# Optimization experiments

Hardware: AMD Instinct MI355X
Metric: run time of the kernel (lower is better)

Reference implementation:

```python
import jax, jax.numpy as jnp
import numpy as np

B = 4096
INPUT_DIM = 4096
N_BLOCKS = 8
BLOCK = INPUT_DIM // N_BLOCKS  # 512
N_EXPERTS = 6
H = 1024   # expert_hidden
H2 = H // 2


def setup_inputs() -> dict:
    key = jax.random.key(0)
    ks = jax.random.split(key, 16)
    s = 0.02  # init scale keeps tanh/softmax in sane range
    return {
        "x":   jax.random.normal(ks[0], (B, INPUT_DIM), jnp.float32),
        # routers: per-block stacked weights [8, ...]
        "Wr1": jax.random.normal(ks[1], (N_BLOCKS, BLOCK, 32), jnp.float32) * s,
        "br1": jax.random.normal(ks[2], (N_BLOCKS, 32), jnp.float32) * s,
        "Wr2": jax.random.normal(ks[3], (N_BLOCKS, 32, N_EXPERTS), jnp.float32) * s,
        "br2": jax.random.normal(ks[4], (N_BLOCKS, N_EXPERTS), jnp.float32) * s,
        # experts: stacked [6, ...], shared across all 8 blocks
        "We1": jax.random.normal(ks[5], (N_EXPERTS, BLOCK, H), jnp.float32) * s,
        "be1": jax.random.normal(ks[6], (N_EXPERTS, H), jnp.float32) * s,
        "We2": jax.random.normal(ks[7], (N_EXPERTS, H, H2), jnp.float32) * s,
        "be2": jax.random.normal(ks[8], (N_EXPERTS, H2), jnp.float32) * s,
        "We3": jax.random.normal(ks[9], (N_EXPERTS, H2, 3), jnp.float32) * s,
        "be3": jax.random.normal(ks[10], (N_EXPERTS, 3), jnp.float32) * s,
        # aggregator
        "Wa1": jax.random.normal(ks[11], (3, 16), jnp.float32) * s,
        "ba1": jax.random.normal(ks[12], (16,), jnp.float32) * s,
        "Wa2": jax.random.normal(ks[13], (16, 3), jnp.float32) * s,
        "ba2": jax.random.normal(ks[14], (3,), jnp.float32) * s,
    }


def reference(x, Wr1, br1, Wr2, br2, We1, be1, We2, be2, We3, be3,
              Wa1, ba1, Wa2, ba2):
    b = x.shape[0]
    blocks = x.reshape(b, N_BLOCKS, BLOCK)                       # [b,s,d]
    # routers (one per block s)
    r1 = jax.nn.relu(jnp.einsum('bsd,sdh->bsh', blocks, Wr1) + br1)
    routing = jax.nn.softmax(
        jnp.einsum('bsh,she->bse', r1, Wr2) + br2, axis=-1)      # [b,s,E]
    # experts applied to every block (grouped GEMMs)
    h1 = jnp.tanh(jnp.einsum('bsd,edh->bseh', blocks, We1) + be1)        # [b,s,E,H]
    h2 = jnp.tanh(jnp.einsum('bseh,ehk->bsek', h1, We2) + be2)           # [b,s,E,H2]
    eo = jnp.einsum('bsek,eko->bseo', h2, We3) + be3                     # [b,s,E,3]
    weighted = jnp.einsum('bse,bseo->bso', routing, eo)                  # [b,s,3]
    final = weighted.mean(axis=1)                                        # mean over 8 blocks
    a1 = jax.nn.relu(final @ Wa1 + ba1)
    return a1 @ Wa2 + ba2                                                # [b,3]
```

## Files before the change

kernel.cpp:

```cpp
#include <hip/hip_runtime.h>
#include <cstdint>
#include <cstddef>

typedef __bf16 bf16;
typedef __bf16 bf16x4 __attribute__((ext_vector_type(4)));
typedef __bf16 bf16x8 __attribute__((ext_vector_type(8)));
typedef float  f32x4  __attribute__((ext_vector_type(4)));
typedef long long i64v;

#define NROWS   32768
#define DBLK    512
#define H1N     1024
#define H2N     512
#define NEXP    6
#define NBATCH  4096
#define HALL    (NEXP * H1N)
#define W2SCALE 32.0f
#define W2INV   0.03125f

__device__ __forceinline__ void gld16(const void* g, void* l) {
    __builtin_amdgcn_global_load_lds(
        (const __attribute__((address_space(1))) void*)g,
        (__attribute__((address_space(3))) void*)l, 16, 0, 0);
}

__device__ __forceinline__ float fast_tanh(float x) {
    float e = __builtin_amdgcn_exp2f(x * 2.8853900817779268f);
    float r = __builtin_amdgcn_rcpf(e + 1.0f);
    return __builtin_fmaf(-2.0f, r, 1.0f);
}

__device__ __forceinline__ float hsum16(float v) {
    v += __shfl_xor(v, 1);
    v += __shfl_xor(v, 2);
    v += __shfl_xor(v, 4);
    v += __shfl_xor(v, 8);
    return v;
}

__device__ __forceinline__ int swz(int row, int g) {
    return row * 64 + ((g ^ (row & 7)) * 8);
}
__device__ __forceinline__ int swz8(int row, int g) {
    return row * 64 + ((g ^ ((row >> 1) & 3)) << 4);
}


__global__ void cvt_bf16_kernel(const float* __restrict__ in,
                                bf16* __restrict__ out, int n4) {
    int i = blockIdx.x * blockDim.x + threadIdx.x;
    if (i >= n4) return;
    float4 v = ((const float4*)in)[i];
    bf16x4 o;
    o.x = (bf16)v.x; o.y = (bf16)v.y; o.z = (bf16)v.z; o.w = (bf16)v.w;
    ((bf16x4*)out)[i] = o;
}

__global__ __launch_bounds__(256) void transpose_cvt(
    const float* __restrict__ in, bf16* __restrict__ out, int K, int N) {
    __shared__ bf16 tile[64][66];
    int e  = blockIdx.z;
    int n0 = blockIdx.x * 64;
    int k0 = blockIdx.y * 64;
    int c  = threadIdx.x & 63;
    int rb = threadIdx.x >> 6;
    const float* src = in + (size_t)e * K * N;
    bf16* dst = out + (size_t)e * N * K;
#pragma unroll
    for (int it = 0; it < 16; ++it) {
        int k = k0 + rb + it * 4;
        int n = n0 + c;
        if (k < K && n < N) tile[rb + it * 4][c] = (bf16)src[(size_t)k * N + n];
    }
    __syncthreads();
#pragma unroll
    for (int it = 0; it < 16; ++it) {
        int n = n0 + rb + it * 4;
        int k = k0 + c;
        if (n < N && k < K) dst[(size_t)n * K + k] = tile[c][rb + it * 4];
    }
}

__global__ __launch_bounds__(256) void transpose_cvt_fp8(
    const float* __restrict__ in, uint8_t* __restrict__ out, int K, int N,
    float scale) {
    __shared__ float tile[64][65];
    int e  = blockIdx.z;
    int n0 = blockIdx.x * 64;
    int k0 = blockIdx.y * 64;
    int c  = threadIdx.x & 63;
    int rb = threadIdx.x >> 6;
    const float* src = in + (size_t)e * K * N;
    uint8_t* dst = out + (size_t)e * N * K;
#pragma unroll
    for (int it = 0; it < 16; ++it) {
        int k = k0 + rb + it * 4;
        int n = n0 + c;
        if (k < K && n < N) tile[rb + it * 4][c] = src[(size_t)k * N + n];
    }
    __syncthreads();
#pragma unroll
    for (int it = 0; it < 16; ++it) {
        int n = n0 + rb + it * 4;
        int k = k0 + c;
        if (n < N && k < K) {
            float v = tile[c][rb + it * 4] * scale;
            int p = __builtin_amdgcn_cvt_pk_fp8_f32(v, v, 0, false);
            dst[(size_t)n * K + k] = (uint8_t)(p & 0xff);
        }
    }
}

__global__ void zero_f32_kernel(float* __restrict__ p, int n) {
    int i = blockIdx.x * blockDim.x + threadIdx.x;
    if (i < n) p[i] = 0.0f;
}


__global__ __launch_bounds__(256, 2) void router_kernel(
    const bf16* __restrict__ xbf,
    const bf16* __restrict__ Wr1t,
    const float* __restrict__ br1,
    const float* __restrict__ Wr2,
    const float* __restrict__ br2,
    float* __restrict__ routing) {
    __shared__ __align__(16) bf16 sA[128 * 64];
    __shared__ __align__(16) bf16 sB[32 * 64];
    const int tid = threadIdx.x;
    const int w = tid >> 6, l = tid & 63;
    const int s  = blockIdx.y;
    const int b0 = blockIdx.x * 128;
    const int wm = w * 32;
    const int srow = l >> 3, schk = (l & 7) * 8;
    const int fr = l & 15, fq = l >> 4;
    const bf16* Ab = xbf + (size_t)s * 512;
    const bf16* Bb = Wr1t + (size_t)s * (32 * 512);

    f32x4 acc[2][2];
#pragma unroll
    for (int i = 0; i < 2; ++i)
#pragma unroll
        for (int j = 0; j < 2; ++j) acc[i][j] = (f32x4){0.f, 0.f, 0.f, 0.f};

    for (int k0 = 0; k0 < 512; k0 += 64) {
        __syncthreads();
#pragma unroll
        for (int jj = 0; jj < 4; ++jj) {
            int row = w * 32 + jj * 8;
            gld16(Ab + (size_t)(b0 + row + srow) * 4096 + k0 + schk, sA + row * 64);
        }
        gld16(Bb + (size_t)(w * 8 + srow) * 512 + k0 + schk, sB + w * 8 * 64);
        __syncthreads();
#pragma unroll
        for (int ks = 0; ks < 2; ++ks) {
            bf16x8 af[2], bfr[2];
#pragma unroll
            for (int i = 0; i < 2; ++i)
                af[i] = *(const bf16x8*)&sA[(wm + i * 16 + fr) * 64 + ks * 32 + fq * 8];
#pragma unroll
            for (int j = 0; j < 2; ++j)
                bfr[j] = *(const bf16x8*)&sB[(j * 16 + fr) * 64 + ks * 32 + fq * 8];
#pragma unroll
            for (int i = 0; i < 2; ++i)
#pragma unroll
                for (int j = 0; j < 2; ++j)
                    acc[i][j] = __builtin_amdgcn_mfma_f32_16x16x32_bf16(
                        af[i], bfr[j], acc[i][j], 0, 0, 0);
        }
    }

    float b1v[2], w2v[2][6], br2v[6];
#pragma unroll
    for (int j = 0; j < 2; ++j) {
        int col = j * 16 + fr;
        b1v[j] = br1[s * 32 + col];
#pragma unroll
        for (int e2 = 0; e2 < 6; ++e2) w2v[j][e2] = Wr2[(s * 32 + col) * 6 + e2];
    }
#pragma unroll
    for (int e2 = 0; e2 < 6; ++e2) br2v[e2] = br2[s * 6 + e2];

#pragma unroll
    for (int i = 0; i < 2; ++i) {
#pragma unroll
        for (int r = 0; r < 4; ++r) {
            float lg[6] = {0.f, 0.f, 0.f, 0.f, 0.f, 0.f};
#pragma unroll
            for (int j = 0; j < 2; ++j) {
                float t = fmaxf(acc[i][j][r] + b1v[j], 0.f);
#pragma unroll
                for (int e2 = 0; e2 < 6; ++e2) lg[e2] += t * w2v[j][e2];
            }
#pragma unroll
            for (int e2 = 0; e2 < 6; ++e2) lg[e2] = hsum16(lg[e2]) + br2v[e2];
            float mx = lg[0];
#pragma unroll
            for (int e2 = 1; e2 < 6; ++e2) mx = fmaxf(mx, lg[e2]);
            float p[6], sum = 0.f;
#pragma unroll
            for (int e2 = 0; e2 < 6; ++e2) { p[e2] = __expf(lg[e2] - mx); sum += p[e2]; }
            float inv = __fdividef(1.f, sum);
            if (fr == 0) {
                int brow = b0 + wm + i * 16 + fq * 4 + r;
                float* dst = routing + ((size_t)brow * 8 + s) * 6;
#pragma unroll
                for (int e2 = 0; e2 < 6; ++e2) dst[e2] = p[e2] * inv;
            }
        }
    }
}

__global__ __launch_bounds__(512, 2) void gemm1_kernel(
    const bf16* __restrict__ A,
    const bf16* __restrict__ B,
    const float* __restrict__ bias,
    uint8_t* __restrict__ h1,
    int ldh) {
    __shared__ __align__(16) bf16 sA[2][256 * 64];
    __shared__ __align__(16) bf16 sB[2][256 * 64];
    const int tid = threadIdx.x;
    const int w = tid >> 6, l = tid & 63;
    const int n0 = blockIdx.x * 256;
    const int m0 = blockIdx.y * 256;
    const int wm = (w & 1) * 128;
    const int wn = (w >> 1) * 64;
    const int fr = l & 15, fq = l >> 4;

    const int rbase = w * 32 + (l >> 3);
    const int gg = l & 7;
    const bf16* Ag = A + (size_t)(m0 + rbase) * DBLK + gg * 8;
    const bf16* Bg = B + (size_t)(n0 + rbase) * DBLK + gg * 8;
    const int woff = rbase * 64 + ((gg ^ (l >> 3)) * 8);

    f32x4 acc[8][4];
#pragma unroll
    for (int i = 0; i < 8; ++i)
#pragma unroll
        for (int j = 0; j < 4; ++j) acc[i][j] = (f32x4){0.f, 0.f, 0.f, 0.f};

#define G1_LOAD(SA_, SB_, T_)                                              \
    {                                                                      \
        _Pragma("unroll") for (int q = 0; q < 4; ++q) {                    \
            SA_[q] = *(const bf16x8*)(Ag + (size_t)q * 4096 + (T_) * 64);  \
            SB_[q] = *(const bf16x8*)(Bg + (size_t)q * 4096 + (T_) * 64);  \
        }                                                                  \
    }
#define G1_WRITE(SA_, SB_, BUF_)                                           \
    {                                                                      \
        _Pragma("unroll") for (int q = 0; q < 4; ++q) {                    \
            *(bf16x8*)&sA[BUF_][woff + q * 512] = SA_[q];                  \
            *(bf16x8*)&sB[BUF_][woff + q * 512] = SB_[q];                  \
        }                                                                  \
    }
#define G1_COMP(BUF_)                                                      \
    {                                                                      \
        _Pragma("unroll") for (int ks = 0; ks < 2; ++ks) {                 \
            bf16x8 af[8], bfr[4];                                          \
            _Pragma("unroll") for (int i = 0; i < 8; ++i)                  \
                af[i] = *(const bf16x8*)&sA[BUF_][swz(wm + i * 16 + fr,    \
                                                      ks * 4 + fq)];       \
            _Pragma("unroll") for (int j = 0; j < 4; ++j)                  \
                bfr[j] = *(const bf16x8*)&sB[BUF_][swz(wn + j * 16 + fr,   \
                                                       ks * 4 + fq)];      \
            __builtin_amdgcn_s_setprio(1);                                 \
            _Pragma("unroll") for (int i = 0; i < 8; ++i)                  \
                _Pragma("unroll") for (int j = 0; j < 4; ++j)              \
                    acc[i][j] = __builtin_amdgcn_mfma_f32_16x16x32_bf16(   \
                        af[i], bfr[j], acc[i][j], 0, 0, 0);                \
            __builtin_amdgcn_s_setprio(0);                                 \
        }                                                                  \
    }
#define G1_BAR()                                                           \
    asm volatile("s_waitcnt lgkmcnt(0)" ::: "memory");                     \
    __builtin_amdgcn_s_barrier();                                          \
    __builtin_amdgcn_sched_barrier(0);

    bf16x8 S0A[4], S0B[4], S1A[4], S1B[4];
    G1_LOAD(S0A, S0B, 0)
    G1_LOAD(S1A, S1B, 1)
    G1_WRITE(S0A, S0B, 0)
    G1_BAR()
    G1_LOAD(S0A, S0B, 2) G1_WRITE(S1A, S1B, 1) G1_COMP(0) G1_BAR()
    G1_LOAD(S1A, S1B, 3) G1_WRITE(S0A, S0B, 0) G1_COMP(1) G1_BAR()
    G1_LOAD(S0A, S0B, 4) G1_WRITE(S1A, S1B, 1) G1_COMP(0) G1_BAR()
    G1_LOAD(S1A, S1B, 5) G1_WRITE(S0A, S0B, 0) G1_COMP(1) G1_BAR()
    G1_LOAD(S0A, S0B, 6) G1_WRITE(S1A, S1B, 1) G1_COMP(0) G1_BAR()
    G1_LOAD(S1A, S1B, 7) G1_WRITE(S0A, S0B, 0) G1_COMP(1) G1_BAR()
    G1_WRITE(S1A, S1B, 1) G1_COMP(0) G1_BAR()
    G1_COMP(1)

#undef G1_LOAD
#undef G1_WRITE
#undef G1_COMP
#undef G1_BAR

    float4 bb[8];
#pragma unroll
    for (int i = 0; i < 8; ++i)
        bb[i] = *(const float4*)&bias[m0 + wm + i * 16 + fq * 4];
#pragma unroll
    for (int j = 0; j < 4; ++j) {
        int xrow = n0 + wn + j * 16 + fr;
        uint8_t* dst = &h1[(size_t)xrow * ldh + m0 + wm + fq * 4];
#pragma unroll
        for (int i = 0; i < 8; ++i) {
            float t0 = fast_tanh(acc[i][j][0] + bb[i].x);
            float t1 = fast_tanh(acc[i][j][1] + bb[i].y);
            float t2 = fast_tanh(acc[i][j][2] + bb[i].z);
            float t3 = fast_tanh(acc[i][j][3] + bb[i].w);
            int p = 0;
            p = __builtin_amdgcn_cvt_pk_fp8_f32(t0, t1, p, false);
            p = __builtin_amdgcn_cvt_pk_fp8_f32(t2, t3, p, true);
            *(uint32_t*)(dst + i * 16) = (uint32_t)p;
        }
    }
}

__global__ __launch_bounds__(256, 4) void gemm2_kernel(
    const uint8_t* __restrict__ h1,
    const uint8_t* __restrict__ W2f8t,
    const float* __restrict__ be2,
    const float* __restrict__ We3,
    float* __restrict__ eo,
    int ldh) {
    __shared__ __align__(16) uint8_t sA[128 * 64];
    __shared__ __align__(16) uint8_t sB[128 * 64];
    __shared__ float w3s[128 * 3];
    __shared__ float b2s[128];
    const int tid = threadIdx.x;
    const int w = tid >> 6, l = tid & 63;
    const int e  = blockIdx.z;
    const int n0 = blockIdx.x * 128;
    const int m0 = blockIdx.y * 128;
    const int wm = (w & 1) * 64, wn = (w >> 1) * 64;
    const int srow4 = l >> 2;
    const int g4 = (((l & 3) ^ ((l >> 3) & 3)) << 4);
    const int fr = l & 15, fq = l >> 4;
    const uint8_t* Ae = W2f8t + (size_t)e * (H2N * H1N);
    const uint8_t* Be = h1 + (size_t)e * H1N;

    if (tid < 128) {
        int c = m0 + tid;
        b2s[tid] = be2[e * H2N + c];
        w3s[tid * 3 + 0] = We3[((size_t)e * H2N + c) * 3 + 0];
        w3s[tid * 3 + 1] = We3[((size_t)e * H2N + c) * 3 + 1];
        w3s[tid * 3 + 2] = We3[((size_t)e * H2N + c) * 3 + 2];
    }

    f32x4 acc[4][4];
#pragma unroll
    for (int i = 0; i < 4; ++i)
#pragma unroll
        for (int j = 0; j < 4; ++j) acc[i][j] = (f32x4){0.f, 0.f, 0.f, 0.f};

    for (int k0 = 0; k0 < H1N; k0 += 64) {
        __syncthreads();
#pragma unroll
        for (int jj = 0; jj < 2; ++jj) {
            int row = w * 32 + jj * 16 + srow4;
            gld16(Ae + (size_t)(m0 + row) * H1N + k0 + g4, sA + (w * 32 + jj * 16) * 64);
            gld16(Be + (size_t)(n0 + row) * ldh + k0 + g4, sB + (w * 32 + jj * 16) * 64);
        }
        __syncthreads();
#pragma unroll
        for (int ks = 0; ks < 2; ++ks) {
            i64v af[4], bfr[4];
#pragma unroll
            for (int i = 0; i < 4; ++i) {
                int row = wm + i * 16 + fr;
                af[i] = *(const i64v*)&sA[swz8(row, ks * 2 + (fq >> 1)) + ((fq & 1) << 3)];
            }
#pragma unroll
            for (int j = 0; j < 4; ++j) {
                int row = wn + j * 16 + fr;
                bfr[j] = *(const i64v*)&sB[swz8(row, ks * 2 + (fq >> 1)) + ((fq & 1) << 3)];
            }
#pragma unroll
            for (int i = 0; i < 4; ++i)
#pragma unroll
                for (int j = 0; j < 4; ++j)
                    acc[i][j] = __builtin_amdgcn_mfma_f32_16x16x32_fp8_fp8(
                        af[i], bfr[j], acc[i][j], 0, 0, 0);
        }
    }

    float p[4][3];
#pragma unroll
    for (int j = 0; j < 4; ++j) { p[j][0] = 0.f; p[j][1] = 0.f; p[j][2] = 0.f; }
#pragma unroll
    for (int i = 0; i < 4; ++i) {
        int cl = wm + i * 16 + fq * 4;
        float4 bb = *(const float4*)&b2s[cl];
        float4 wa = *(const float4*)&w3s[cl * 3 + 0];
        float4 wb = *(const float4*)&w3s[cl * 3 + 4];
        float4 wc = *(const float4*)&w3s[cl * 3 + 8];
        float bias4[4] = {bb.x, bb.y, bb.z, bb.w};
        float w30[4] = {wa.x, wa.w, wb.z, wc.y};
        float w31[4] = {wa.y, wb.x, wb.w, wc.z};
        float w32[4] = {wa.z, wb.y, wc.x, wc.w};
#pragma unroll
        for (int j = 0; j < 4; ++j) {
#pragma unroll
            for (int r = 0; r < 4; ++r) {
                float t = fast_tanh(acc[i][j][r] * W2INV + bias4[r]);
                p[j][0] += t * w30[r];
                p[j][1] += t * w31[r];
                p[j][2] += t * w32[r];
            }
        }
    }
#pragma unroll
    for (int j = 0; j < 4; ++j) {
        float v0 = p[j][0], v1 = p[j][1], v2 = p[j][2];
        v0 += __shfl_xor(v0, 16); v0 += __shfl_xor(v0, 32);
        v1 += __shfl_xor(v1, 16); v1 += __shfl_xor(v1, 32);
        v2 += __shfl_xor(v2, 16); v2 += __shfl_xor(v2, 32);
        if (fq == 0) {
            int xrow = n0 + wn + j * 16 + fr;
            float* dst = eo + ((size_t)e * NROWS + xrow) * 3;
            atomicAdd(dst + 0, v0);
            atomicAdd(dst + 1, v1);
            atomicAdd(dst + 2, v2);
        }
    }
}

__global__ void final_kernel(
    const float* __restrict__ routing, const float* __restrict__ eo,
    const float* __restrict__ be3, const float* __restrict__ Wa1,
    const float* __restrict__ ba1, const float* __restrict__ Wa2,
    const float* __restrict__ ba2, float* __restrict__ out) {
    int b = blockIdx.x * blockDim.x + threadIdx.x;
    if (b >= NBATCH) return;
    float f0 = 0.f, f1 = 0.f, f2 = 0.f;
    for (int s = 0; s < 8; ++s) {
        int r = b * 8 + s;
        const float* rt = routing + (size_t)r * 6;
#pragma unroll
        for (int e = 0; e < 6; ++e) {
            float wgt = rt[e];
            const float* eop = eo + ((size_t)e * NROWS + r) * 3;
            f0 += wgt * (eop[0] + be3[e * 3 + 0]);
            f1 += wgt * (eop[1] + be3[e * 3 + 1]);
            f2 += wgt * (eop[2] + be3[e * 3 + 2]);
        }
    }
    f0 *= 0.125f; f1 *= 0.125f; f2 *= 0.125f;
    float o0 = ba2[0], o1 = ba2[1], o2 = ba2[2];
#pragma unroll
    for (int h = 0; h < 16; ++h) {
        float a = f0 * Wa1[h] + f1 * Wa1[16 + h] + f2 * Wa1[32 + h] + ba1[h];
        a = fmaxf(a, 0.f);
        o0 += a * Wa2[h * 3 + 0];
        o1 += a * Wa2[h * 3 + 1];
        o2 += a * Wa2[h * 3 + 2];
    }
    out[b * 3 + 0] = o0;
    out[b * 3 + 1] = o1;
    out[b * 3 + 2] = o2;
}


extern "C" void kernel_launch(void* const* d_in, const int* in_sizes, int n_in,
                              void* d_out, int out_size, void* d_ws, size_t ws_size,
                              hipStream_t stream) {
    const float* x   = (const float*)d_in[0];
    const float* Wr1 = (const float*)d_in[1];
    const float* br1 = (const float*)d_in[2];
    const float* Wr2 = (const float*)d_in[3];
    const float* br2 = (const float*)d_in[4];
    const float* We1 = (const float*)d_in[5];
    const float* be1 = (const float*)d_in[6];
    const float* We2 = (const float*)d_in[7];
    const float* be2 = (const float*)d_in[8];
    const float* We3 = (const float*)d_in[9];
    const float* be3 = (const float*)d_in[10];
    const float* Wa1 = (const float*)d_in[11];
    const float* ba1 = (const float*)d_in[12];
    const float* Wa2 = (const float*)d_in[13];
    const float* ba2 = (const float*)d_in[14];
    float* out = (float*)d_out;

    char* ws = (char*)d_ws;
    const size_t off_xbf  = 0;
    const size_t off_w1t  = off_xbf  + (size_t)33554432;
    const size_t off_w2t  = off_w1t  + (size_t)6291456;
    const size_t off_wr1t = off_w2t  + (size_t)6291456;
    const size_t off_rout = off_wr1t + (size_t)262144;
    const size_t off_eo   = off_rout + (size_t)786432;
    const size_t off_h1   = off_eo   + (size_t)2359296;

    if (off_h1 + (size_t)NROWS * HALL > ws_size) return;

    bf16*    xbf     = (bf16*)(ws + off_xbf);
    bf16*    W1t     = (bf16*)(ws + off_w1t);
    uint8_t* W2f8t   = (uint8_t*)(ws + off_w2t);
    bf16*    Wr1t    = (bf16*)(ws + off_wr1t);
    float*   routing = (float*)(ws + off_rout);
    float*   eo      = (float*)(ws + off_eo);
    uint8_t* h1      = (uint8_t*)(ws + off_h1);

    cvt_bf16_kernel<<<16384, 256, 0, stream>>>(x, xbf, 4194304);
    transpose_cvt<<<dim3(16, 8, 6), 256, 0, stream>>>(We1, W1t, 512, 1024);
    transpose_cvt_fp8<<<dim3(8, 16, 6), 256, 0, stream>>>(We2, W2f8t, 1024, 512, W2SCALE);
    transpose_cvt<<<dim3(1, 8, 8), 256, 0, stream>>>(Wr1, Wr1t, 512, 32);
    zero_f32_kernel<<<2304, 256, 0, stream>>>(eo, 589824);

    router_kernel<<<dim3(32, 8), 256, 0, stream>>>(xbf, Wr1t, br1, Wr2, br2, routing);

    gemm1_kernel<<<dim3(NROWS / 256, HALL / 256), 512, 0, stream>>>(
        W1t, xbf, be1, h1, HALL);
    gemm2_kernel<<<dim3(NROWS / 128, H2N / 128, NEXP), 256, 0, stream>>>(
        h1, W2f8t, be2, We3, eo, HALL);

    final_kernel<<<16, 256, 0, stream>>>(routing, eo, be3, Wa1, ba1, Wa2, ba2, out);
}
```

Baseline: 661.5 us.

## Pipeline gemm1 with direct global-to-LDS loads and four-phase MFMA interleave

Measured after the change: 657.3 us. About the same (-0.6%).

```diff
diff --git a/kernel.cpp b/kernel.cpp
--- a/kernel.cpp
+++ b/kernel.cpp
@@ -226,11 +226,10 @@
     const int wn = (w >> 1) * 64;
     const int fr = l & 15, fq = l >> 4;
 
-    const int rbase = w * 32 + (l >> 3);
+    const int srow = l >> 3;
     const int gg = l & 7;
-    const bf16* Ag = A + (size_t)(m0 + rbase) * DBLK + gg * 8;
-    const bf16* Bg = B + (size_t)(n0 + rbase) * DBLK + gg * 8;
-    const int woff = rbase * 64 + ((gg ^ (l >> 3)) * 8);
+    const bf16* Ag = A + (size_t)(m0 + w * 32 + srow) * DBLK + ((gg ^ srow) * 8);
+    const bf16* Bg = B + (size_t)(n0 + w * 32 + srow) * DBLK + ((gg ^ srow) * 8);
 
     f32x4 acc[8][4];
 #pragma unroll
@@ -238,61 +237,70 @@
 #pragma unroll
         for (int j = 0; j < 4; ++j) acc[i][j] = (f32x4){0.f, 0.f, 0.f, 0.f};
 
-#define G1_LOAD(SA_, SB_, T_)                                              \
-    {                                                                      \
-        _Pragma("unroll") for (int q = 0; q < 4; ++q) {                    \
-            SA_[q] = *(const bf16x8*)(Ag + (size_t)q * 4096 + (T_) * 64);  \
-            SB_[q] = *(const bf16x8*)(Bg + (size_t)q * 4096 + (T_) * 64);  \
-        }                                                                  \
-    }
-#define G1_WRITE(SA_, SB_, BUF_)                                           \
-    {                                                                      \
-        _Pragma("unroll") for (int q = 0; q < 4; ++q) {                    \
-            *(bf16x8*)&sA[BUF_][woff + q * 512] = SA_[q];                  \
-            *(bf16x8*)&sB[BUF_][woff + q * 512] = SB_[q];                  \
-        }                                                                  \
-    }
-#define G1_COMP(BUF_)                                                      \
-    {                                                                      \
-        _Pragma("unroll") for (int ks = 0; ks < 2; ++ks) {                 \
-            bf16x8 af[8], bfr[4];                                          \
-            _Pragma("unroll") for (int i = 0; i < 8; ++i)                  \
-                af[i] = *(const bf16x8*)&sA[BUF_][swz(wm + i * 16 + fr,    \
-                                                      ks * 4 + fq)];       \
-            _Pragma("unroll") for (int j = 0; j < 4; ++j)                  \
-                bfr[j] = *(const bf16x8*)&sB[BUF_][swz(wn + j * 16 + fr,   \
-                                                       ks * 4 + fq)];      \
-            __builtin_amdgcn_s_setprio(1);                                 \
-            _Pragma("unroll") for (int i = 0; i < 8; ++i)                  \
-                _Pragma("unroll") for (int j = 0; j < 4; ++j)              \
-                    acc[i][j] = __builtin_amdgcn_mfma_f32_16x16x32_bf16(   \
-                        af[i], bfr[j], acc[i][j], 0, 0, 0);                \
-            __builtin_amdgcn_s_setprio(0);                                 \
-        }                                                                  \
-    }
-#define G1_BAR()                                                           \
-    asm volatile("s_waitcnt lgkmcnt(0)" ::: "memory");                     \
-    __builtin_amdgcn_s_barrier();                                          \
+    bf16x8 bfr[4][2];
+
+#pragma unroll
+    for (int q = 0; q < 4; ++q) {
+        gld16(Ag + (size_t)q * 8 * DBLK, &sA[0][(w * 32 + q * 8) * 64]);
+        gld16(Bg + (size_t)q * 8 * DBLK, &sB[0][(w * 32 + q * 8) * 64]);
+        gld16(Bg + (size_t)q * 8 * DBLK + 64, &sB[1][(w * 32 + q * 8) * 64]);
+    }
+    asm volatile("s_waitcnt vmcnt(0)" ::: "memory");
+    __builtin_amdgcn_s_barrier();
     __builtin_amdgcn_sched_barrier(0);
 
-    bf16x8 S0A[4], S0B[4], S1A[4], S1B[4];
-    G1_LOAD(S0A, S0B, 0)
-    G1_LOAD(S1A, S1B, 1)
-    G1_WRITE(S0A, S0B, 0)
-    G1_BAR()
-    G1_LOAD(S0A, S0B, 2) G1_WRITE(S1A, S1B, 1) G1_COMP(0) G1_BAR()
-    G1_LOAD(S1A, S1B, 3) G1_WRITE(S0A, S0B, 0) G1_COMP(1) G1_BAR()
-    G1_LOAD(S0A, S0B, 4) G1_WRITE(S1A, S1B, 1) G1_COMP(0) G1_BAR()
-    G1_LOAD(S1A, S1B, 5) G1_WRITE(S0A, S0B, 0) G1_COMP(1) G1_BAR()
-    G1_LOAD(S0A, S0B, 6) G1_WRITE(S1A, S1B, 1) G1_COMP(0) G1_BAR()
-    G1_LOAD(S1A, S1B, 7) G1_WRITE(S0A, S0B, 0) G1_COMP(1) G1_BAR()
-    G1_WRITE(S1A, S1B, 1) G1_COMP(0) G1_BAR()
-    G1_COMP(1)
-
-#undef G1_LOAD
-#undef G1_WRITE
-#undef G1_COMP
-#undef G1_BAR
+#define G1_PHASE(TAU, P)                                                      \
+    {                                                                         \
+        constexpr int CUR_ = (TAU) & 1;                                       \
+        if constexpr ((P) == 0 && (TAU) < 7) {                                \
+            _Pragma("unroll") for (int q = 0; q < 4; ++q)                     \
+                gld16(Ag + (size_t)q * 8 * DBLK + ((TAU) + 1) * 64,           \
+                      &sA[1 - CUR_][(w * 32 + q * 8) * 64]);                  \
+        }                                                                     \
+        if constexpr ((P) == 1 && (TAU) < 6) {                                \
+            _Pragma("unroll") for (int q = 0; q < 4; ++q)                     \
+                gld16(Bg + (size_t)q * 8 * DBLK + ((TAU) + 2) * 64,           \
+                      &sB[CUR_][(w * 32 + q * 8) * 64]);                      \
+        }                                                                     \
+        if constexpr ((P) == 0) {                                             \
+            _Pragma("unroll") for (int j = 0; j < 4; ++j)                     \
+                _Pragma("unroll") for (int ks = 0; ks < 2; ++ks)              \
+                    bfr[j][ks] = *(const bf16x8*)&sB[CUR_][                   \
+                        swz(wn + j * 16 + fr, ks * 4 + fq)];                  \
+        }                                                                     \
+        bf16x8 af0 = *(const bf16x8*)&sA[CUR_][swz(wm + (P)*32 + fr, fq)];    \
+        bf16x8 af1 = *(const bf16x8*)&sA[CUR_][swz(wm + (P)*32 + fr, 4 + fq)];\
+        bf16x8 af2 = *(const bf16x8*)&sA[CUR_][swz(wm + (P)*32 + 16 + fr, fq)];\
+        bf16x8 af3 = *(const bf16x8*)&sA[CUR_][swz(wm + (P)*32 + 16 + fr, 4 + fq)];\
+        asm volatile("s_waitcnt lgkmcnt(0)" ::: "memory");                    \
+        __builtin_amdgcn_sched_barrier(0);                                    \
+        __builtin_amdgcn_s_setprio(1);                                        \
+        _Pragma("unroll") for (int j = 0; j < 4; ++j) {                       \
+            acc[(P)*2][j] = __builtin_amdgcn_mfma_f32_16x16x32_bf16(          \
+                af0, bfr[j][0], acc[(P)*2][j], 0, 0, 0);                      \
+            acc[(P)*2][j] = __builtin_amdgcn_mfma_f32_16x16x32_bf16(          \
+                af1, bfr[j][1], acc[(P)*2][j], 0, 0, 0);                      \
+            acc[(P)*2 + 1][j] = __builtin_amdgcn_mfma_f32_16x16x32_bf16(      \
+                af2, bfr[j][0], acc[(P)*2 + 1][j], 0, 0, 0);                  \
+            acc[(P)*2 + 1][j] = __builtin_amdgcn_mfma_f32_16x16x32_bf16(      \
+                af3, bfr[j][1], acc[(P)*2 + 1][j], 0, 0, 0);                  \
+        }                                                                     \
+        __builtin_amdgcn_s_setprio(0);                                        \
+        if constexpr ((P) == 3 && (TAU) < 6)                                  \
+            asm volatile("s_waitcnt vmcnt(4)" ::: "memory");                  \
+        if constexpr ((P) == 3 && (TAU) == 6)                                 \
+            asm volatile("s_waitcnt vmcnt(0)" ::: "memory");                  \
+        __builtin_amdgcn_s_barrier();                                         \
+        __builtin_amdgcn_sched_barrier(0);                                    \
+    }
+#define G1_TILE(TAU) \
+    G1_PHASE(TAU, 0) G1_PHASE(TAU, 1) G1_PHASE(TAU, 2) G1_PHASE(TAU, 3)
+
+    G1_TILE(0) G1_TILE(1) G1_TILE(2) G1_TILE(3)
+    G1_TILE(4) G1_TILE(5) G1_TILE(6) G1_TILE(7)
+
+#undef G1_PHASE
+#undef G1_TILE
 
     float4 bb[8];
 #pragma unroll
```
